# Optimization experiments

Measured on AMD Instinct MI355X. Metric: run time of the kernel, lower is better.

The kernel has to match this reference:

```python
import jax, jax.numpy as jnp
import numpy as np

B, V, K, H, HID = 512, 50000, 200, 300, 800
BETA, EPSILON = 0.5, 1.0
REAL_MIN = 1e-30


def setup_inputs() -> dict:
    key = jax.random.key(0)
    ks = jax.random.split(key, 6)
    bows = jax.random.randint(ks[0], (B, V), 0, 5).astype(jnp.float32)
    # scale embeddings so inner products are O(1) and exp() stays in range
    rho = jax.random.normal(ks[1], (V, H), dtype=jnp.float32) * 0.05
    alpha = jax.random.normal(ks[2], (K, H), dtype=jnp.float32) * 0.05
    W1 = jax.random.normal(ks[3], (V, HID), dtype=jnp.float32) * (1.0 / np.sqrt(V))
    b1 = jnp.zeros((HID,), dtype=jnp.float32)
    W2 = jax.random.normal(ks[4], (HID, K), dtype=jnp.float32) * (1.0 / np.sqrt(HID))
    b2 = jnp.zeros((K,), dtype=jnp.float32)
    return {"bows": bows, "rho": rho, "alpha": alpha, "W1": W1, "b1": b1, "W2": W2, "b2": b2}


def _forward(bows, rho, alpha, W1, b1, W2, b2):
    # Infer_Net: 2-layer MLP, relu hidden, softplus output -> positive theta (B, K)
    hid = jax.nn.relu(bows @ W1 + b1)
    theta = jax.nn.softplus(hid @ W2 + b2)

    inner = rho @ alpha.T                                  # (V, K)
    dis = jnp.clip(jnp.exp(inner), 1e-30, 1e10)            # dis_d in torch code
    cost = jnp.clip(jnp.exp(-inner), 1e-30, 1e10)          # cost_c
    theta_norm = jax.nn.softmax(theta, axis=-1)            # (B, K)

    # --- _cost_ct, vectorized over docs using counts instead of ragged token lists ---
    # token list of doc d = each word w repeated bows[d, w] times, so every per-token
    # gather/normalize/sum collapses to counts-weighted dense reductions.
    cd = cost * dis                                        # (V, K)
    n_tok = bows.sum(axis=1)                               # (B,) tokens per doc
    valid = n_tok > 0

    # forward: per (word, doc) f = sum_k cost*dis*theta / (sum_k dis*theta + eps)
    num = cd @ theta_norm.T                                # (V, B)
    den = dis @ theta_norm.T                               # (V, B)
    f = num / (den + REAL_MIN)                             # (V, B)
    fwd_per_doc = jnp.einsum('bv,vb->b', bows, f) / jnp.maximum(n_tok, 1.0)
    forward_cost = jnp.where(valid, fwd_per_doc, 0.0).sum()

    # backward: column (topic) normalization weighted by counts
    colsum = bows @ dis                                    # (B, K) = sum_w c_dw * dis[w,k]
    A = bows @ cd                                          # (B, K) = sum_w c_dw * cost*dis
    bwd_per_doc = (A / (colsum + REAL_MIN) * theta_norm).sum(axis=1)
    backward_cost = jnp.where(valid, bwd_per_doc, 0.0).sum()

    # --- Poisson reconstruction (tm_cost) ---
    phi = jax.nn.softmax(inner, axis=0)                    # softmax over vocab dim
    recon = (phi @ theta.T).T                              # (B, V)
    tm = -(bows * jnp.log(recon + 1e-10) - recon - jax.lax.lgamma(bows + 1.0)).sum(-1).mean()

    return jnp.stack([EPSILON * tm, BETA * forward_cost, (1.0 - BETA) * backward_cost])


def reference(bows, rho, alpha, W1, b1, W2, b2):
    return _forward(bows, rho, alpha, W1, b1, W2, b2)
```

## Files before the change

kernel.cpp:

```cpp
#include <hip/hip_runtime.h>

#define B_    512
#define V_    50000
#define VP    50048
#define KT    200
#define HH    300
#define HIDN  800
#define KP    224
#define HP    320
#define NVB   782
#define ZG1   32
#define NF    1024

typedef __attribute__((ext_vector_type(4))) float  f32x4;
typedef __attribute__((ext_vector_type(8))) short  s8v;
typedef __attribute__((ext_vector_type(8))) __bf16 bf16x8;
typedef unsigned int u32;

static __device__ __forceinline__ f32x4 mfma16(s8v a, s8v b, f32x4 c){
  return __builtin_amdgcn_mfma_f32_16x16x32_bf16(
      __builtin_bit_cast(bf16x8, a), __builtin_bit_cast(bf16x8, b), c, 0, 0, 0);
}
static __device__ __forceinline__ short f2bf(float f){
  unsigned u = __float_as_uint(f);
  u = (u + 0x7fffu + ((u >> 16) & 1u)) >> 16;
  return (short)u;
}
static __device__ __forceinline__ void load_lds16(const short* g, short* lds){
  __builtin_amdgcn_global_load_lds(
      (const __attribute__((address_space(1))) u32*)g,
      (__attribute__((address_space(3))) u32*)lds, 16, 0, 0);
}
static __device__ __forceinline__ float lgtab(float x){
  return x < 1.5f ? 0.f : (x < 2.5f ? 0.69314718056f :
         (x < 3.5f ? 1.79175946923f : 3.17805383035f));
}

__global__ void kzero(float* p, long n){
  long i = blockIdx.x * (long)blockDim.x + threadIdx.x;
  long st = (long)gridDim.x * blockDim.x;
  for(; i < n; i += st) p[i] = 0.f;
}

__global__ __launch_bounds__(256) void k_bows(const float* __restrict__ src,
                                              short* __restrict__ dst,
                                              float* __restrict__ ntok_acc,
                                              float* __restrict__ lg_acc){
  __shared__ float r4[4], g4[4];
  int b = blockIdx.y;
  int c = blockIdx.x * 256 + threadIdx.x;
  int lane = threadIdx.x & 63, w = threadIdx.x >> 6;
  float s = 0.f, gs = 0.f;
  if(c < VP / 8){
    int v = c * 8;
    s8v o = {0,0,0,0,0,0,0,0};
    if(v + 8 <= V_){
      float4 a = *(const float4*)&src[(long)b * V_ + v];
      float4 d = *(const float4*)&src[(long)b * V_ + v + 4];
      o[0]=f2bf(a.x); o[1]=f2bf(a.y); o[2]=f2bf(a.z); o[3]=f2bf(a.w);
      o[4]=f2bf(d.x); o[5]=f2bf(d.y); o[6]=f2bf(d.z); o[7]=f2bf(d.w);
      s = a.x + a.y + a.z + a.w + d.x + d.y + d.z + d.w;
      gs = lgtab(a.x)+lgtab(a.y)+lgtab(a.z)+lgtab(a.w)
         + lgtab(d.x)+lgtab(d.y)+lgtab(d.z)+lgtab(d.w);
    }
    *(s8v*)&dst[(long)b * VP + v] = o;
  }
  #pragma unroll
  for(int k = 32; k >= 1; k >>= 1){ s += __shfl_xor(s, k, 64); gs += __shfl_xor(gs, k, 64); }
  if(lane == 0){ r4[w] = s; g4[w] = gs; }
  __syncthreads();
  if(threadIdx.x == 0){
    atomicAdd(&ntok_acc[b], r4[0] + r4[1] + r4[2] + r4[3]);
    atomicAdd(&lg_acc[b],   g4[0] + g4[1] + g4[2] + g4[3]);
  }
}

__global__ __launch_bounds__(256) void k_transW1(const float* __restrict__ W1,
                                                 short* __restrict__ W1t){
  __shared__ float tile[32][33];
  int v0 = blockIdx.x * 32, n0 = blockIdx.y * 32;
  int tid = threadIdx.x;
  int r = tid >> 3, c4 = (tid & 7) * 4;
  float4 val = {0.f,0.f,0.f,0.f};
  int v = v0 + r;
  if(v < V_) val = *(const float4*)&W1[(long)v * HIDN + n0 + c4];
  tile[r][c4+0] = val.x; tile[r][c4+1] = val.y; tile[r][c4+2] = val.z; tile[r][c4+3] = val.w;
  __syncthreads();
  short4 o;
  o.x = f2bf(tile[c4+0][r]); o.y = f2bf(tile[c4+1][r]);
  o.z = f2bf(tile[c4+2][r]); o.w = f2bf(tile[c4+3][r]);
  *(short4*)&W1t[(long)(n0 + r) * VP + v0 + c4] = o;
}

__global__ __launch_bounds__(256) void k_transW2(const float* __restrict__ W2,
                                                 short* __restrict__ W2t){
  __shared__ float tile[32][33];
  int h0 = blockIdx.x * 32, t0 = blockIdx.y * 32;
  int tid = threadIdx.x;
  int r = tid >> 3, c4 = (tid & 7) * 4;
  #pragma unroll
  for(int j = 0; j < 4; j++){
    int t = t0 + c4 + j;
    tile[r][c4+j] = (t < KT) ? W2[(long)(h0 + r) * KT + t] : 0.f;
  }
  __syncthreads();
  short4 o;
  o.x = f2bf(tile[c4+0][r]); o.y = f2bf(tile[c4+1][r]);
  o.z = f2bf(tile[c4+2][r]); o.w = f2bf(tile[c4+3][r]);
  *(short4*)&W2t[(long)(t0 + r) * HIDN + h0 + c4] = o;
}

__global__ void kconvpad(const float* __restrict__ src, short* __restrict__ dst,
                         int kin, int kpad){
  int r = blockIdx.x, c = threadIdx.x;
  float v = (c < kin) ? src[(long)r * kin + c] : 0.f;
  dst[(long)r * kpad + c] = f2bf(v);
}

__global__ __launch_bounds__(256) void k_gemmf(const short* __restrict__ Ab,
                                               const short* __restrict__ Bb,
                                               float* __restrict__ Chid,
                                               float* __restrict__ Ccol){
  __shared__ short As[2][128 * 32];
  __shared__ short Bs[2][128 * 32];
  int tid = threadIdx.x, w = tid >> 6, lane = tid & 63, lm = lane & 15, q = lane >> 4;
  int f = blockIdx.x;
  int lid = (f & 7) * 128 + (f >> 3);
  int z = lid >> 5, rem = lid & 31;
  int by = rem >> 2, bx = rem & 3;
  int m0 = bx * 128, n0 = by * 128;
  long kstart = (long)z * 1568;
  long kend = kstart + 1568; if(kend > VP) kend = VP;
  int rsub = lane >> 2;
  int kl = (((lane & 3) ^ ((lane >> 3) & 3))) * 8;
  int rA0 = m0 + w * 16 + rsub;
  int rA1 = m0 + (w + 4) * 16 + rsub;
  int nB0 = n0 + w * 16 + rsub;
  int nB1 = n0 + (w + 4) * 16 + rsub;
  int qx = (q ^ ((lm >> 1) & 3)) * 8;
  int wr = (w >> 1) * 64, wc = (w & 1) * 64;
  f32x4 acc[4][4];
  #pragma unroll
  for(int i = 0; i < 4; i++)
    #pragma unroll
    for(int j = 0; j < 4; j++) acc[i][j] = (f32x4){0.f,0.f,0.f,0.f};

  auto STAGE = [&](int buf, long kb){
    load_lds16(&Ab[(long)rA0 * VP + kb + kl], &As[buf][w * 512]);
    load_lds16(&Ab[(long)rA1 * VP + kb + kl], &As[buf][(w + 4) * 512]);
    load_lds16(&Bb[(long)nB0 * VP + kb + kl], &Bs[buf][w * 512]);
    load_lds16(&Bb[(long)nB1 * VP + kb + kl], &Bs[buf][(w + 4) * 512]);
  };

  STAGE(0, kstart);
  __syncthreads();
  int cur = 0;
  for(long kb = kstart; kb < kend; kb += 32){
    if(kb + 32 < kend) STAGE(cur ^ 1, kb + 32);
    s8v af[4], bfr[4];
    #pragma unroll
    for(int i = 0; i < 4; i++) af[i]  = *(const s8v*)&As[cur][(wr + i * 16 + lm) * 32 + qx];
    #pragma unroll
    for(int j = 0; j < 4; j++) bfr[j] = *(const s8v*)&Bs[cur][(wc + j * 16 + lm) * 32 + qx];
    #pragma unroll
    for(int i = 0; i < 4; i++)
      #pragma unroll
      for(int j = 0; j < 4; j++)
        acc[i][j] = mfma16(af[i], bfr[j], acc[i][j]);
    __syncthreads();
    cur ^= 1;
  }
  float* cp = Chid + (long)z * B_ * HIDN;
  float* cc = Ccol + (long)z * B_ * KP;
  #pragma unroll
  for(int i = 0; i < 4; i++)
    #pragma unroll
    for(int j = 0; j < 4; j++){
      int gm = m0 + wr + i * 16 + q * 4;
      int gn = n0 + wc + j * 16 + lm;
      if(gn < HIDN){
        #pragma unroll
        for(int r = 0; r < 4; r++) cp[(long)(gm + r) * HIDN + gn] = acc[i][j][r];
      } else {
        int t = gn - HIDN;
        #pragma unroll
        for(int r = 0; r < 4; r++) cc[(long)(gm + r) * KP + t] = acc[i][j][r];
      }
    }
}

__global__ __launch_bounds__(256) void k_hidred(const float* __restrict__ hid_part,
                                                const float* __restrict__ b1,
                                                short* __restrict__ hid_b){
  int idx = blockIdx.x * 256 + threadIdx.x;
  if(idx >= B_ * HIDN / 4) return;
  int b = idx / (HIDN / 4), hc = (idx % (HIDN / 4)) * 4;
  float4 acc = *(const float4*)&b1[hc];
  #pragma unroll 8
  for(int z = 0; z < ZG1; z++){
    float4 v = *(const float4*)&hid_part[((long)z * B_ + b) * HIDN + hc];
    acc.x += v.x; acc.y += v.y; acc.z += v.z; acc.w += v.w;
  }
  short4 o;
  o.x = f2bf(fmaxf(acc.x, 0.f)); o.y = f2bf(fmaxf(acc.y, 0.f));
  o.z = f2bf(fmaxf(acc.z, 0.f)); o.w = f2bf(fmaxf(acc.w, 0.f));
  *(short4*)&hid_b[(long)b * HIDN + hc] = o;
}

__global__ __launch_bounds__(256) void k_gemm2(const short* __restrict__ Ab,
                                               const short* __restrict__ Bb,
                                               float* __restrict__ C){
  __shared__ short As[2][128 * 32];
  __shared__ short Bs[2][128 * 32];
  int tid = threadIdx.x, w = tid >> 6, lane = tid & 63, lm = lane & 15, q = lane >> 4;
  int m0 = blockIdx.x * 128, n0 = blockIdx.y * 128;
  int rsub = lane >> 2;
  int kl = (((lane & 3) ^ ((lane >> 3) & 3))) * 8;
  int rA0 = m0 + w * 16 + rsub;
  int rA1 = m0 + (w + 4) * 16 + rsub;
  int nB0 = n0 + w * 16 + rsub;       if(nB0 > KP - 1) nB0 = KP - 1;
  int nB1 = n0 + (w + 4) * 16 + rsub; if(nB1 > KP - 1) nB1 = KP - 1;
  int qx = (q ^ ((lm >> 1) & 3)) * 8;
  int wr = (w >> 1) * 64, wc = (w & 1) * 64;
  f32x4 acc[4][4];
  #pragma unroll
  for(int i = 0; i < 4; i++)
    #pragma unroll
    for(int j = 0; j < 4; j++) acc[i][j] = (f32x4){0.f,0.f,0.f,0.f};

  auto STAGE = [&](int buf, long kb){
    load_lds16(&Ab[(long)rA0 * HIDN + kb + kl], &As[buf][w * 512]);
    load_lds16(&Ab[(long)rA1 * HIDN + kb + kl], &As[buf][(w + 4) * 512]);
    load_lds16(&Bb[(long)nB0 * HIDN + kb + kl], &Bs[buf][w * 512]);
    load_lds16(&Bb[(long)nB1 * HIDN + kb + kl], &Bs[buf][(w + 4) * 512]);
  };

  STAGE(0, 0);
  __syncthreads();
  int cur = 0;
  for(long kb = 0; kb < HIDN; kb += 32){
    if(kb + 32 < HIDN) STAGE(cur ^ 1, kb + 32);
    s8v af[4], bfr[4];
    #pragma unroll
    for(int i = 0; i < 4; i++) af[i]  = *(const s8v*)&As[cur][(wr + i * 16 + lm) * 32 + qx];
    #pragma unroll
    for(int j = 0; j < 4; j++) bfr[j] = *(const s8v*)&Bs[cur][(wc + j * 16 + lm) * 32 + qx];
    #pragma unroll
    for(int i = 0; i < 4; i++)
      #pragma unroll
      for(int j = 0; j < 4; j++)
        acc[i][j] = mfma16(af[i], bfr[j], acc[i][j]);
    __syncthreads();
    cur ^= 1;
  }
  #pragma unroll
  for(int i = 0; i < 4; i++)
    #pragma unroll
    for(int j = 0; j < 4; j++){
      int gm = m0 + wr + i * 16 + q * 4;
      int gn = n0 + wc + j * 16 + lm;
      if(gn < KP){
        #pragma unroll
        for(int r = 0; r < 4; r++) C[(long)(gm + r) * KP + gn] = acc[i][j][r];
      }
    }
}

__global__ __launch_bounds__(256) void k_thpost(const float* __restrict__ theta_z,
                                                const float* __restrict__ b2,
                                                const float* __restrict__ sumexp,
                                                short* __restrict__ thetas_b,
                                                short* __restrict__ thetan_b,
                                                float* __restrict__ thetan_f,
                                                float* __restrict__ theta_sum){
  __shared__ float thl[256];
  __shared__ float redm[4], reds[4], redt[4];
  int b = blockIdx.x, tid = threadIdx.x;
  float th = 0.f;
  if(tid < KT){
    float zz = theta_z[(long)b * KP + tid] + b2[tid];
    th = (zz > 0.f ? zz : 0.f) + log1pf(expf(-fabsf(zz)));
  }
  thl[tid] = (tid < KT) ? th : -1e30f;
  __syncthreads();
  float m = thl[tid];
  #pragma unroll
  for(int s = 32; s >= 1; s >>= 1) m = fmaxf(m, __shfl_xor(m, s, 64));
  if((tid & 63) == 0) redm[tid >> 6] = m;
  __syncthreads();
  float mx = fmaxf(fmaxf(redm[0], redm[1]), fmaxf(redm[2], redm[3]));
  float e  = (tid < KT) ? expf(th - mx) : 0.f;
  float ts_ = (tid < KT) ? th : 0.f;
  float s_ = e;
  #pragma unroll
  for(int s = 32; s >= 1; s >>= 1){ s_ += __shfl_xor(s_, s, 64); ts_ += __shfl_xor(ts_, s, 64); }
  if((tid & 63) == 0){ reds[tid >> 6] = s_; redt[tid >> 6] = ts_; }
  __syncthreads();
  float sum = reds[0] + reds[1] + reds[2] + reds[3];
  if(tid < KP){
    short ts  = (tid < KT) ? f2bf(th / sumexp[tid]) : (short)0;
    short tnb = (tid < KT) ? f2bf(e / sum) : (short)0;
    thetas_b[(long)b * KP + tid] = ts;
    thetan_b[(long)b * KP + tid] = tnb;
  }
  if(tid < KT) thetan_f[(long)b * KT + tid] = e / sum;
  if(tid == 0) theta_sum[b] = redt[0] + redt[1] + redt[2] + redt[3];
}

__global__ __launch_bounds__(256) void k_inner(const short* __restrict__ rho_p,
                                               const short* __restrict__ alpha_p,
                                               short* __restrict__ dis_t,
                                               short* __restrict__ dis_v,
                                               float* __restrict__ sumexp){
  __shared__ short As[128 * 40];
  __shared__ short Bs[64 * 40];
  __shared__ short tDis[128 * 72];
  __shared__ float sume_l[64];
  int tid = threadIdx.x, w = tid >> 6, lane = tid & 63, lm = lane & 15, q = lane >> 4;
  int v0 = blockIdx.x * 128, t0 = blockIdx.y * 64;
  if(tid < 64) sume_l[tid] = 0.f;
  __syncthreads();
  f32x4 acc[2][4];
  #pragma unroll
  for(int i = 0; i < 2; i++)
    #pragma unroll
    for(int j = 0; j < 4; j++) acc[i][j] = (f32x4){0.f,0.f,0.f,0.f};

  for(int h0 = 0; h0 < HP; h0 += 32){
    #pragma unroll
    for(int c0 = 0; c0 < 2; c0++){
      int c = tid + c0 * 256;
      int r = c >> 2, off = (c & 3) * 8;
      int vg = v0 + r;
      s8v v = {0,0,0,0,0,0,0,0};
      if(vg < V_) v = *(const s8v*)&rho_p[(long)vg * HP + h0 + off];
      *(s8v*)&As[r * 40 + off] = v;
    }
    {
      int r = tid >> 2, off = (tid & 3) * 8;
      int tg = t0 + r;
      s8v v = {0,0,0,0,0,0,0,0};
      if(tg < KT) v = *(const s8v*)&alpha_p[(long)tg * HP + h0 + off];
      *(s8v*)&Bs[r * 40 + off] = v;
    }
    __syncthreads();
    s8v af[2], bfr[4];
    #pragma unroll
    for(int i = 0; i < 2; i++) af[i]  = *(const s8v*)&As[(w * 32 + i * 16 + lm) * 40 + q * 8];
    #pragma unroll
    for(int j = 0; j < 4; j++) bfr[j] = *(const s8v*)&Bs[(j * 16 + lm) * 40 + q * 8];
    #pragma unroll
    for(int i = 0; i < 2; i++)
      #pragma unroll
      for(int j = 0; j < 4; j++)
        acc[i][j] = mfma16(af[i], bfr[j], acc[i][j]);
    __syncthreads();
  }
  #pragma unroll
  for(int i = 0; i < 2; i++)
    #pragma unroll
    for(int j = 0; j < 4; j++){
      int tg = t0 + j * 16 + lm;
      float s4 = 0.f;
      #pragma unroll
      for(int r = 0; r < 4; r++){
        int vloc = w * 32 + i * 16 + q * 4 + r;
        int vg = v0 + vloc;
        float x = acc[i][j][r];
        float e1 = __expf(x);  e1 = fminf(fmaxf(e1, 1e-30f), 1e10f);
        bool valid = (vg < V_) && (tg < KT);
        float dv = valid ? e1 : 0.f;
        tDis[vloc * 72 + (j * 16 + lm)] = f2bf(dv);
        s4 += dv;
      }
      s4 += __shfl_xor(s4, 16, 64);
      s4 += __shfl_xor(s4, 32, 64);
      if(q == 0) atomicAdd(&sume_l[j * 16 + lm], s4);
    }
  __syncthreads();
  for(int c = tid; c < 1024; c += 256){
    int t = c & 63, vch = c >> 6;
    int tg = t0 + t;
    if(tg < KP){
      s8v d;
      #pragma unroll
      for(int j = 0; j < 8; j++) d[j] = tDis[(vch * 8 + j) * 72 + t];
      *(s8v*)&dis_t[(long)tg * VP + v0 + vch * 8] = d;
    }
  }
  for(int c = tid; c < 1024; c += 256){
    int r = c >> 3, tch = (c & 7) * 8;
    if(t0 + tch < KP)
      *(s8v*)&dis_v[(long)(v0 + r) * KP + t0 + tch] = *(const s8v*)&tDis[r * 72 + tch];
  }
  if(tid < 64 && (t0 + tid) < KT) atomicAdd(&sumexp[t0 + tid], sume_l[tid]);
}

__global__ __launch_bounds__(256) void k_consumer(const short* __restrict__ dis_v,
                                                  const short* __restrict__ thetan_b,
                                                  const short* __restrict__ thetas_b,
                                                  const short* __restrict__ bows_b,
                                                  float* __restrict__ fwd_part,
                                                  float* __restrict__ tm_part){
  __shared__ short tTN[64 * 256];
  __shared__ short tTS[64 * 256];
  __shared__ float fwd_lw[4][64];
  __shared__ float tm_lw[4];
  int tid = threadIdx.x;
  int w = tid >> 6, lane = tid & 63, lm = lane & 15, q = lane >> 4;
  int bx = blockIdx.x, by = blockIdx.y;
  int v0 = bx * 64;
  #pragma unroll
  for(int t = 0; t < 8; t++){
    int g = (t << 8) + tid;
    int doc = g >> 5;
    int pb = (g & 31) << 4;
    int sb = (doc & 7) << 4;
    long src = (long)(by * 64 + doc) * KP + ((pb ^ sb) >> 1);
    long lim = (long)B_ * KP - 8;
    if(src > lim) src = lim;
    short* dN = &tTN[(long)(((t << 2) + w) << 9)];
    short* dS = &tTS[(long)(((t << 2) + w) << 9)];
    load_lds16(&thetan_b[src], dN);
    load_lds16(&thetas_b[src], dS);
  }
  int vrow = v0 + w * 16 + lm;
  s8v disf[7];
  #pragma unroll
  for(int i = 0; i < 7; i++)
    disf[i] = *(const s8v*)&dis_v[(long)vrow * KP + i * 32 + q * 8];
  short4 bw4[4];
  #pragma unroll
  for(int cb = 0; cb < 4; cb++){
    int bg = by * 64 + cb * 16 + lm;
    bw4[cb] = *(const short4*)&bows_b[(long)bg * VP + v0 + w * 16 + q * 4];
  }
  __syncthreads();
  int sl = (lm & 7) << 4;
  float tmreg = 0.f;
  #pragma unroll
  for(int cb = 0; cb < 4; cb++){
    int rowb = (cb * 16 + lm) << 8;
    f32x4 aD = {0.f,0.f,0.f,0.f}, aR = {0.f,0.f,0.f,0.f};
    #pragma unroll
    for(int i = 0; i < 7; i++){
      int off = rowb + ((((i << 6) + (q << 4)) ^ sl) >> 1);
      s8v tn = *(const s8v*)&tTN[off];
      s8v ts = *(const s8v*)&tTS[off];
      aD = mfma16(disf[i], tn, aD);
      aR = mfma16(disf[i], ts, aR);
    }
    float fwd_p = 0.f;
    #pragma unroll
    for(int r = 0; r < 4; r++){
      float bv = __uint_as_float(((unsigned)(unsigned short)(&bw4[cb].x)[r]) << 16);
      float den = aD[r] + 1e-30f;
      float rec = aR[r];
      fwd_p += bv * __builtin_amdgcn_rcpf(den);
      tmreg += bv * __log2f(rec + 1e-10f);
    }
    fwd_p += __shfl_xor(fwd_p, 16, 64); fwd_p += __shfl_xor(fwd_p, 32, 64);
    if(q == 0) fwd_lw[w][cb * 16 + lm] = fwd_p;
  }
  #pragma unroll
  for(int s = 32; s >= 1; s >>= 1) tmreg += __shfl_xor(tmreg, s, 64);
  if(lane == 0) tm_lw[w] = tmreg;
  __syncthreads();
  if(tid < 64)
    fwd_part[(long)(by * 64 + tid) * NVB + bx] =
      fwd_lw[0][tid] + fwd_lw[1][tid] + fwd_lw[2][tid] + fwd_lw[3][tid];
  if(tid == 0)
    tm_part[(long)by * NVB + bx] =
      0.69314718056f * (tm_lw[0] + tm_lw[1] + tm_lw[2] + tm_lw[3]);
}

__global__ __launch_bounds__(64) void k_bwd(const float* __restrict__ colsum_part,
                                            const float* __restrict__ thn_f,
                                            const float* __restrict__ fwd_part,
                                            const float* __restrict__ ntok_acc,
                                            float* __restrict__ bwd_pd,
                                            float* __restrict__ fwd_pd){
  int b = blockIdx.x, lane = threadIdx.x;
  float s = 0.f;
  for(int t = lane; t < KT; t += 64){
    float cs = 0.f;
    #pragma unroll 8
    for(int z = 0; z < ZG1; z++) cs += colsum_part[((long)z * B_ + b) * KP + t];
    s += thn_f[(long)b * KT + t] * __builtin_amdgcn_rcpf(cs + 1e-30f);
  }
  float fp = 0.f;
  for(int p = lane; p < NVB; p += 64) fp += fwd_part[(long)b * NVB + p];
  #pragma unroll
  for(int k = 32; k >= 1; k >>= 1){ s += __shfl_xor(s, k, 64); fp += __shfl_xor(fp, k, 64); }
  if(lane == 0){
    float nt = ntok_acc[b];
    bwd_pd[b] = s * nt;
    fwd_pd[b] = fp / fmaxf(nt, 1.f);
  }
}

__global__ __launch_bounds__(512) void k_final(const float* __restrict__ bwd_pd,
                                               const float* __restrict__ fwd_pd,
                                               const float* __restrict__ ntok_acc,
                                               const float* __restrict__ tm_part,
                                               const float* __restrict__ theta_sum,
                                               const float* __restrict__ lg_acc,
                                               float* __restrict__ out){
  __shared__ float rf[8], rb[8], rt[8];
  int tid = threadIdx.x, w = tid >> 6, lane = tid & 63;
  bool valid = ntok_acc[tid] > 0.f;
  float fw = valid ? fwd_pd[tid] : 0.f;
  float bw = valid ? bwd_pd[tid] : 0.f;
  float tl = 0.f;
  for(int i = tid; i < 8 * NVB; i += 512) tl += tm_part[i];
  float tc = theta_sum[tid] + lg_acc[tid] - tl;
  #pragma unroll
  for(int s = 32; s >= 1; s >>= 1){
    fw += __shfl_xor(fw, s, 64); bw += __shfl_xor(bw, s, 64); tc += __shfl_xor(tc, s, 64);
  }
  if(lane == 0){ rf[w] = fw; rb[w] = bw; rt[w] = tc; }
  __syncthreads();
  if(tid == 0){
    float F = 0.f, Bw = 0.f, T = 0.f;
    #pragma unroll
    for(int i = 0; i < 8; i++){ F += rf[i]; Bw += rb[i]; T += rt[i]; }
    out[0] = T / (float)B_;
    out[1] = 0.5f * F;
    out[2] = 0.5f * Bw;
  }
}

extern "C" void kernel_launch(void* const* d_in, const int* in_sizes, int n_in,
                              void* d_out, int out_size, void* d_ws, size_t ws_size,
                              hipStream_t stream){
  const float* bows  = (const float*)d_in[0];
  const float* rho   = (const float*)d_in[1];
  const float* alpha = (const float*)d_in[2];
  const float* W1    = (const float*)d_in[3];
  const float* b1    = (const float*)d_in[4];
  const float* W2    = (const float*)d_in[5];
  const float* b2    = (const float*)d_in[6];
  float* out = (float*)d_out;
  char* ws = (char*)d_ws;
  size_t o = 0;
  auto alloc = [&](size_t bytes) -> char* {
    char* p = ws + o; o = (o + bytes + 255) & ~(size_t)255; return p;
  };
  float* sumexp     = (float*)alloc(KP * 4);
  float* ntok_acc   = (float*)alloc(B_ * 4);
  float* lg_acc     = (float*)alloc(B_ * 4);
  float* bwd_pd     = (float*)alloc(B_ * 4);
  float* fwd_pd     = (float*)alloc(B_ * 4);
  size_t zbytes = o;
  short* bows_b     = (short*)alloc((size_t)B_ * VP * 2);
  short* Bcomb      = (short*)alloc((size_t)NF * VP * 2);
  short* W1t        = Bcomb;
  short* dis_t      = Bcomb + (size_t)HIDN * VP;
  short* W2t        = (short*)alloc((size_t)KP * HIDN * 2);
  short* rho_p      = (short*)alloc((size_t)V_ * HP * 2);
  short* alpha_p    = (short*)alloc((size_t)KT * HP * 2);
  short* hid_b      = (short*)alloc((size_t)B_ * HIDN * 2);
  float* theta_z    = (float*)alloc((size_t)B_ * KP * 4);
  short* thetas_b   = (short*)alloc((size_t)B_ * KP * 2);
  short* thetan_b   = (short*)alloc((size_t)B_ * KP * 2);
  float* thetan_f   = (float*)alloc((size_t)B_ * KT * 4);
  float* theta_sum  = (float*)alloc(B_ * 4);
  short* dis_v      = (short*)alloc((size_t)VP * KP * 2);
  float* fwd_part   = (float*)alloc((size_t)B_ * NVB * 4);
  float* tm_part    = (float*)alloc((size_t)8 * NVB * 4);
  float* hid_part   = (float*)alloc((size_t)ZG1 * B_ * HIDN * 4);
  float* colsum_part= (float*)alloc((size_t)ZG1 * B_ * KP * 4);

  kzero<<<8, 256, 0, stream>>>((float*)ws, (long)(zbytes / 4));
  k_bows<<<dim3(25, 512), 256, 0, stream>>>(bows, bows_b, ntok_acc, lg_acc);
  k_transW1<<<dim3(VP / 32, HIDN / 32), 256, 0, stream>>>(W1, W1t);
  k_transW2<<<dim3(HIDN / 32, KP / 32), 256, 0, stream>>>(W2, W2t);
  kconvpad<<<V_, HP, 0, stream>>>(rho, rho_p, HH, HP);
  kconvpad<<<KT, HP, 0, stream>>>(alpha, alpha_p, HH, HP);
  k_inner<<<dim3(VP / 128, 4), 256, 0, stream>>>(rho_p, alpha_p, dis_t, dis_v, sumexp);
  k_gemmf<<<dim3(1024), 256, 0, stream>>>(bows_b, Bcomb, hid_part, colsum_part);
  k_hidred<<<dim3(B_ * HIDN / 4 / 256), 256, 0, stream>>>(hid_part, b1, hid_b);
  k_gemm2<<<dim3(4, 2), 256, 0, stream>>>(hid_b, W2t, theta_z);
  k_thpost<<<B_, 256, 0, stream>>>(theta_z, b2, sumexp, thetas_b, thetan_b,
                                   thetan_f, theta_sum);
  k_consumer<<<dim3(NVB, 8), 256, 0, stream>>>(dis_v, thetan_b, thetas_b, bows_b,
                                               fwd_part, tm_part);
  k_bwd<<<B_, 64, 0, stream>>>(colsum_part, thetan_f, fwd_part, ntok_acc, bwd_pd, fwd_pd);
  k_final<<<1, 512, 0, stream>>>(bwd_pd, fwd_pd, ntok_acc, tm_part, theta_sum, lg_acc, out);
}
```

Baseline: 646.5 us.

## Give each wave private LDS staging in k_gemmf to drop block barriers

Restructures the k_gemmf tile so each wave owns a 32x128 output slice. Each wave stages its own A rows and the full B tile into private double-buffered LDS regions, and uses explicit vmcnt waits instead of __syncthreads. This removes block-wide barriers from the K loop. In exchange, every wave loads the full B tile, so global and LDS traffic for B rises fourfold and LDS use grows, which may lower occupancy.

Measured after the change: 684.1 us. +5.8%, slower.

```diff
diff --git a/kernel.cpp b/kernel.cpp
--- a/kernel.cpp
+++ b/kernel.cpp
@@ -121,8 +121,8 @@
                                                const short* __restrict__ Bb,
                                                float* __restrict__ Chid,
                                                float* __restrict__ Ccol){
-  __shared__ short As[2][128 * 32];
-  __shared__ short Bs[2][128 * 32];
+  __shared__ short Aw[4][2][1024];
+  __shared__ short Bw[4][2][4096];
   int tid = threadIdx.x, w = tid >> 6, lane = tid & 63, lm = lane & 15, q = lane >> 4;
   int f = blockIdx.x;
   int lid = (f & 7) * 128 + (f >> 3);
@@ -133,51 +133,51 @@
   long kend = kstart + 1568; if(kend > VP) kend = VP;
   int rsub = lane >> 2;
   int kl = (((lane & 3) ^ ((lane >> 3) & 3))) * 8;
-  int rA0 = m0 + w * 16 + rsub;
-  int rA1 = m0 + (w + 4) * 16 + rsub;
-  int nB0 = n0 + w * 16 + rsub;
-  int nB1 = n0 + (w + 4) * 16 + rsub;
   int qx = (q ^ ((lm >> 1) & 3)) * 8;
-  int wr = (w >> 1) * 64, wc = (w & 1) * 64;
-  f32x4 acc[4][4];
-  #pragma unroll
-  for(int i = 0; i < 4; i++)
-    #pragma unroll
-    for(int j = 0; j < 4; j++) acc[i][j] = (f32x4){0.f,0.f,0.f,0.f};
+  int rA = m0 + w * 32 + rsub;
+  f32x4 acc[2][8];
+  #pragma unroll
+  for(int i = 0; i < 2; i++)
+    #pragma unroll
+    for(int j = 0; j < 8; j++) acc[i][j] = (f32x4){0.f,0.f,0.f,0.f};
 
   auto STAGE = [&](int buf, long kb){
-    load_lds16(&Ab[(long)rA0 * VP + kb + kl], &As[buf][w * 512]);
-    load_lds16(&Ab[(long)rA1 * VP + kb + kl], &As[buf][(w + 4) * 512]);
-    load_lds16(&Bb[(long)nB0 * VP + kb + kl], &Bs[buf][w * 512]);
-    load_lds16(&Bb[(long)nB1 * VP + kb + kl], &Bs[buf][(w + 4) * 512]);
+    load_lds16(&Ab[(long)rA * VP + kb + kl],        &Aw[w][buf][0]);
+    load_lds16(&Ab[(long)(rA + 16) * VP + kb + kl], &Aw[w][buf][512]);
+    #pragma unroll
+    for(int g = 0; g < 8; g++)
+      load_lds16(&Bb[(long)(n0 + g * 16 + rsub) * VP + kb + kl], &Bw[w][buf][g * 512]);
   };
 
   STAGE(0, kstart);
-  __syncthreads();
   int cur = 0;
   for(long kb = kstart; kb < kend; kb += 32){
-    if(kb + 32 < kend) STAGE(cur ^ 1, kb + 32);
-    s8v af[4], bfr[4];
-    #pragma unroll
-    for(int i = 0; i < 4; i++) af[i]  = *(const s8v*)&As[cur][(wr + i * 16 + lm) * 32 + qx];
-    #pragma unroll
-    for(int j = 0; j < 4; j++) bfr[j] = *(const s8v*)&Bs[cur][(wc + j * 16 + lm) * 32 + qx];
-    #pragma unroll
-    for(int i = 0; i < 4; i++)
+    if(kb + 32 < kend){
+      STAGE(cur ^ 1, kb + 32);
+      asm volatile("s_waitcnt vmcnt(10)" ::: "memory");
+    } else {
+      asm volatile("s_waitcnt vmcnt(0)" ::: "memory");
+    }
+    s8v af[2], bfr[8];
+    #pragma unroll
+    for(int i = 0; i < 2; i++) af[i]  = *(const s8v*)&Aw[w][cur][(i * 16 + lm) * 32 + qx];
+    #pragma unroll
+    for(int j = 0; j < 8; j++) bfr[j] = *(const s8v*)&Bw[w][cur][(j * 16 + lm) * 32 + qx];
+    #pragma unroll
+    for(int i = 0; i < 2; i++)
       #pragma unroll
-      for(int j = 0; j < 4; j++)
+      for(int j = 0; j < 8; j++)
         acc[i][j] = mfma16(af[i], bfr[j], acc[i][j]);
-    __syncthreads();
     cur ^= 1;
   }
   float* cp = Chid + (long)z * B_ * HIDN;
   float* cc = Ccol + (long)z * B_ * KP;
   #pragma unroll
-  for(int i = 0; i < 4; i++)
-    #pragma unroll
-    for(int j = 0; j < 4; j++){
-      int gm = m0 + wr + i * 16 + q * 4;
-      int gn = n0 + wc + j * 16 + lm;
+  for(int i = 0; i < 2; i++)
+    #pragma unroll
+    for(int j = 0; j < 8; j++){
+      int gm = m0 + w * 32 + i * 16 + q * 4;
+      int gn = n0 + j * 16 + lm;
       if(gn < HIDN){
         #pragma unroll
         for(int r = 0; r < 4; r++) cp[(long)(gm + r) * HIDN + gn] = acc[i][j][r];
```
